# Kernel tuning notes

Measured on AMD Instinct MI355X. Metric: run time of the kernel, lower is better.

Reference implementation:

```python
import jax, jax.numpy as jnp
import numpy as np

B, N, D, P = 32, 16, 64, 8  # batch, num_objs, in_feat_dim, patch size
PAIRS = N * (N - 1)


def _conv_relu(x, W, b):
    # Conv2d(kernel=3, stride=1, padding=1) + ReLU, NCHW/OIHW layout
    y = jax.lax.conv_general_dilated(
        x, W, window_strides=(1, 1), padding='SAME',
        dimension_numbers=('NCHW', 'OIHW', 'NCHW'))
    return jax.nn.relu(y + b[None, :, None, None])


def setup_inputs() -> dict:
    key = jax.random.key(0)
    ks = jax.random.split(key, 12)
    x = jax.random.normal(ks[0], (B, N, D, P, P), jnp.float32)
    # g_idx: cols 0,1 index into the repeated pair axis of size N*(N-1); col 2 is a 0/1 mask
    i0 = jax.random.randint(ks[1], (B, PAIRS, 1), 0, PAIRS)
    i1 = jax.random.randint(ks[2], (B, PAIRS, 1), 0, PAIRS)
    m = jax.random.randint(ks[3], (B, PAIRS, 1), 0, 2)
    g_idx = jnp.concatenate([i0, i1, m], axis=2)

    def w(k, o, i):
        return jax.random.normal(k, (o, i, 3, 3), jnp.float32) * (1.0 / np.sqrt(i * 9.0))

    return {
        'x': x, 'g_idx': g_idx,
        'W_rel': w(ks[4], D, 2 * D), 'b_rel': jnp.zeros((D,), jnp.float32),
        'W_self': w(ks[5], D, D), 'b_self': jnp.zeros((D,), jnp.float32),
        'W_aff': w(ks[6], D, D), 'b_aff': jnp.zeros((D,), jnp.float32),
        'W_agg': w(ks[7], D, 2 * D), 'b_agg': jnp.zeros((D,), jnp.float32),
    }


def reference(x, g_idx, W_rel, b_rel, W_self, b_self, W_aff, b_aff, W_agg, b_agg):
    b, n, d, p, _ = x.shape
    pairs = n * (n - 1)
    s = x
    # x1: [B, N*(N-1), D, P, P]
    x1 = jnp.tile(x, (1, n - 1, 1, 1, 1))

    def gather_pair(col):
        idx = g_idx[:, :, col][:, :, None, None, None]  # [B, pairs, 1, 1, 1]
        idx = jnp.broadcast_to(idx, (b, pairs, d, p, p))
        return jnp.take_along_axis(x1, idx, axis=1)

    y1 = gather_pair(0)
    y2 = gather_pair(1)
    mask = g_idx[:, :, 2][:, :, None, None, None].astype(x.dtype)
    r = jnp.concatenate([y1, y2], axis=2) * mask  # [B, pairs, 2D, P, P]
    r = _conv_relu(r.reshape(-1, 2 * d, p, p), W_rel, b_rel)
    r = r.reshape(b, n, n - 1, d, p, p).sum(axis=2)  # scatter-sum per object

    xs = _conv_relu(x.reshape(-1, d, p, p), W_self, b_self).reshape(b, n, d, p, p)
    pred = xs + r
    a = _conv_relu(pred.reshape(-1, d, p, p), W_aff, b_aff).reshape(b, n, d, p, p)
    a = jnp.concatenate([a, s], axis=2)  # [B, N, 2D, P, P]
    out = _conv_relu(a.reshape(-1, 2 * d, p, p), W_agg, b_agg).reshape(b, n, d, p, p)
    return out
```

## Files before the change

kernel.cpp:

```cpp
#include <hip/hip_runtime.h>


#define NIMG 512
#define IMGSZ 4096

using bf16x8 = __attribute__((ext_vector_type(8))) short;
using f32x4  = __attribute__((ext_vector_type(4))) float;

__device__ inline unsigned short f2bf(float f) {
  union { float f; unsigned u; } v; v.f = f;
  unsigned r = v.u + 0x7fffu + ((v.u >> 16) & 1u);
  return (unsigned short)(r >> 16);
}

__device__ inline f32x4 bf4_to_f32(uint2 p) {
  union { unsigned u; float f; } c;
  f32x4 r;
  c.u = (p.x & 0xffffu) << 16;  r[0] = c.f;
  c.u = (p.x & 0xffff0000u);    r[1] = c.f;
  c.u = (p.y & 0xffffu) << 16;  r[2] = c.f;
  c.u = (p.y & 0xffff0000u);    r[3] = c.f;
  return r;
}

__global__ __launch_bounds__(256) void prep_w(
    const float* __restrict__ Wr, const float* __restrict__ Ws,
    const float* __restrict__ Wa, const float* __restrict__ Wg,
    unsigned short* __restrict__ Wt)
{
  int i4 = (blockIdx.x * 256 + threadIdx.x) * 4;
  if (i4 >= 221184) return;
  unsigned short o4[4];
#pragma unroll
  for (int e = 0; e < 4; ++e) {
    int idx = i4 + e;
    float v;
    if (idx < 73728) {
      int c = idx / 36864, r = idx % 36864;
      int t = r >> 12, oc = (r >> 6) & 63, ic = r & 63;
      v = (c == 0 ? Ws : Wa)[oc * 576 + ic * 9 + t];
    } else {
      int r2 = idx - 73728;
      int half = r2 / 73728, rr = r2 % 73728;
      int t = rr >> 13, oc = (rr >> 7) & 63, ic = rr & 127;
      v = (half ? Wg : Wr)[oc * 1152 + ic * 9 + t];
    }
    o4[e] = f2bf(v);
  }
  uint2 pk;
  pk.x = (unsigned)o4[0] | ((unsigned)o4[1] << 16);
  pk.y = (unsigned)o4[2] | ((unsigned)o4[3] << 16);
  *(uint2*)(Wt + i4) = pk;
}

__device__ inline void decode_img(int j, int& b, int& o) {
  b = ((j >> 7) << 3) | (j & 7);
  o = (j >> 3) & 15;
}

template<int ROWX>
__device__ inline void stage_x512(const float* __restrict__ xb,
                                  unsigned short* __restrict__ s,
                                  int coff, int w8, int px) {
#pragma unroll
  for (int r = 0; r < 4; ++r) {
    int ic0 = (w8 + 8 * r) * 2;
    const float* sp = xb + ic0 * 64;
    float a = sp[px], c = sp[64 + px];
    *(unsigned*)(s + px * ROWX + coff + ic0) =
        (unsigned)f2bf(a) | ((unsigned)f2bf(c) << 16);
  }
}

__global__ __launch_bounds__(512, 4) void k1(
    const float* __restrict__ x,
    const unsigned short* __restrict__ Wt,
    unsigned short* __restrict__ cA, unsigned short* __restrict__ cB)
{
  constexpr int ROW = 72;
  __shared__ __align__(16) unsigned short sX[65 * ROW];
  int b, o;
  decode_img(blockIdx.x, b, o);
  const int img = b * 16 + o;
  const int tid = threadIdx.x;
  const int w8 = tid >> 6, lane = tid & 63;

  stage_x512<ROW>(x + (size_t)img * IMGSZ, sX, 0, w8, lane);
  if (tid < 36) ((unsigned*)(sX + 64 * ROW))[tid] = 0;
  __syncthreads();

  const int half = tid >> 8;
  const int w = w8 & 3;
  const int q = lane >> 4, n16 = lane & 15;
  const int ocb = w * 16;
  const int co = ocb + q * 4;

  int pyt[4], pxt[4];
#pragma unroll
  for (int t = 0; t < 4; ++t) { int p = t * 16 + n16; pyt[t] = p >> 3; pxt[t] = p & 7; }

  f32x4 acc[4] = {};
  const unsigned short* WH = Wt + 73728 + (ocb + n16) * 128 + q * 8 + half * 64;
#pragma unroll
  for (int tap = 0; tap < 9; ++tap) {
    const int dy = tap / 3 - 1, dx = tap % 3 - 1;
    int spt[4];
#pragma unroll
    for (int t = 0; t < 4; ++t) {
      int sy = pyt[t] + dy, sx = pxt[t] + dx;
      spt[t] = ((unsigned)sy < 8u && (unsigned)sx < 8u) ? (sy * 8 + sx) : 64;
    }
#pragma unroll
    for (int ks = 0; ks < 2; ++ks) {
      bf16x8 aa = *(const bf16x8*)(WH + tap * 8192 + ks * 32);
#pragma unroll
      for (int t = 0; t < 4; ++t) {
        bf16x8 bt = *(const bf16x8*)(sX + spt[t] * ROW + ks * 32 + q * 8);
        acc[t] = __builtin_amdgcn_mfma_f32_16x16x32_bf16(aa, bt, acc[t], 0, 0, 0);
      }
    }
  }

  unsigned short* dst = half ? cB : cA;
  const size_t ib = (size_t)img * IMGSZ;
#pragma unroll
  for (int t = 0; t < 4; ++t) {
    int p = t * 16 + n16;
    uint2 pa;
    pa.x = (unsigned)f2bf(acc[t][0]) | ((unsigned)f2bf(acc[t][1]) << 16);
    pa.y = (unsigned)f2bf(acc[t][2]) | ((unsigned)f2bf(acc[t][3]) << 16);
    *(uint2*)(dst + ib + p * 64 + co) = pa;
  }
}

__global__ __launch_bounds__(512, 4) void k2(
    const float* __restrict__ x,
    const int* __restrict__ g_idx,
    const unsigned short* __restrict__ Wt,
    const float* __restrict__ b_rel, const float* __restrict__ b_self,
    const float* __restrict__ b_aff, const float* __restrict__ b_agg,
    const unsigned short* __restrict__ cA, const unsigned short* __restrict__ cB,
    float* __restrict__ out)
{
  constexpr int ROW = 72, ROW2 = 136, XROW = 68;
  __shared__ __align__(16) unsigned short sX[65 * ROW2];
  __shared__ __align__(16) unsigned short sPred[65 * ROW];
  __shared__ __align__(16) float sXS[64 * XROW];
  __shared__ int so1a[16], so2a[16];
  __shared__ float sma[16];
  __shared__ int s_na;

  int b, i;
  decode_img(blockIdx.x, b, i);
  const int img = b * 16 + i;
  const int tid = threadIdx.x;
  const int w8 = tid >> 6, lane = tid & 63;

  int o1v = 0, o2v = 0, mv = 0;
  if (tid < 15) {
    const int* gp = g_idx + ((size_t)b * 240 + i * 15 + tid) * 3;
    o1v = gp[0] & 15;
    o2v = gp[1] & 15;
    mv  = gp[2];
  }
  if (tid < 64) {
    if (tid < 16) { so1a[tid] = 0; so2a[tid] = 0; sma[tid] = 0.f; }
    unsigned long long mk = __ballot(mv != 0);
    int pfx = (int)__popcll(mk & ((1ull << tid) - 1));
    if (mv) { so1a[pfx] = o1v; so2a[pfx] = o2v; sma[pfx] = 1.f; }
    if (tid == 0) s_na = (int)__popcll(mk);
  }

  stage_x512<ROW2>(x + (size_t)img * IMGSZ, sX, 64, w8, lane);
  if (tid < 68) ((unsigned*)(sX + 64 * ROW2))[tid] = 0;
  if (tid < 36) ((unsigned*)(sPred + 64 * ROW))[tid] = 0;
  __syncthreads();

  const int w = w8 & 3;
  const int q = lane >> 4, n16 = lane & 15;
  const int ocb = w * 16;
  const int co = ocb + q * 4;
  const int aw64  = (ocb + n16) * 64 + q * 8;
  const int aw128 = (ocb + n16) * 128 + q * 8;

  int pyt[4], pxt[4];
#pragma unroll
  for (int t = 0; t < 4; ++t) { int p = t * 16 + n16; pyt[t] = p >> 3; pxt[t] = p & 7; }

  if (tid < 256) {
    f32x4 f[4] = {};
    const unsigned short* WS = Wt + aw64;
#pragma unroll
    for (int tap = 0; tap < 9; ++tap) {
      const int dy = tap / 3 - 1, dx = tap % 3 - 1;
      int spt[4];
#pragma unroll
      for (int t = 0; t < 4; ++t) {
        int sy = pyt[t] + dy, sx = pxt[t] + dx;
        spt[t] = ((unsigned)sy < 8u && (unsigned)sx < 8u) ? (sy * 8 + sx) : 64;
      }
#pragma unroll
      for (int ks = 0; ks < 2; ++ks) {
        bf16x8 a = *(const bf16x8*)(WS + tap * 4096 + ks * 32);
#pragma unroll
        for (int t = 0; t < 4; ++t) {
          bf16x8 bt = *(const bf16x8*)(sX + spt[t] * ROW2 + 64 + ks * 32 + q * 8);
          f[t] = __builtin_amdgcn_mfma_f32_16x16x32_bf16(a, bt, f[t], 0, 0, 0);
        }
      }
    }
#pragma unroll
    for (int t = 0; t < 4; ++t) {
      int p = t * 16 + n16;
      f32x4 vs = f[t];
#pragma unroll
      for (int r = 0; r < 4; ++r) vs[r] = fmaxf(vs[r] + b_self[co + r], 0.f);
      *(f32x4*)(sXS + p * XROW + co) = vs;
    }
  }
  __syncthreads();

  {
    const size_t bb = (size_t)b * 16 * IMGSZ;
    const int na = s_na;
    const int nc = (na + 3) >> 2;
    const float c0 = (float)(15 - na);
#pragma unroll 1
    for (int pass = 0; pass < 2; ++pass) {
      const int e = tid * 4 + pass * 2048;
      const int e_px = e >> 6, e_ic = e & 63;
      f32x4 xv = *(const f32x4*)(sXS + e_px * XROW + e_ic);
      float acc[4], br[4];
#pragma unroll
      for (int r = 0; r < 4; ++r) {
        br[r] = b_rel[e_ic + r];
        acc[r] = xv[r] + c0 * fmaxf(br[r], 0.f);
      }
#pragma unroll 1
      for (int c = 0; c < nc; ++c) {
        uint2 v1[4], v2[4];
#pragma unroll
        for (int jj = 0; jj < 4; ++jj) {
          int j = c * 4 + jj;
          v1[jj] = *(const uint2*)(cA + bb + (size_t)so1a[j] * IMGSZ + e);
          v2[jj] = *(const uint2*)(cB + bb + (size_t)so2a[j] * IMGSZ + e);
        }
#pragma unroll
        for (int jj = 0; jj < 4; ++jj) {
          float s = sma[c * 4 + jj];
          f32x4 a1 = bf4_to_f32(v1[jj]);
          f32x4 a2 = bf4_to_f32(v2[jj]);
#pragma unroll
          for (int r = 0; r < 4; ++r)
            acc[r] += s * fmaxf(a1[r] + a2[r] + br[r], 0.f);
        }
      }
      uint2 pk;
      pk.x = (unsigned)f2bf(acc[0]) | ((unsigned)f2bf(acc[1]) << 16);
      pk.y = (unsigned)f2bf(acc[2]) | ((unsigned)f2bf(acc[3]) << 16);
      *(uint2*)(sPred + e_px * ROW + e_ic) = pk;
    }
  }
  __syncthreads();

  if (tid < 256) {
    f32x4 f[4] = {};
    const unsigned short* WA = Wt + 36864 + aw64;
#pragma unroll
    for (int tap = 0; tap < 9; ++tap) {
      const int dy = tap / 3 - 1, dx = tap % 3 - 1;
      int spt[4];
#pragma unroll
      for (int t = 0; t < 4; ++t) {
        int sy = pyt[t] + dy, sx = pxt[t] + dx;
        spt[t] = ((unsigned)sy < 8u && (unsigned)sx < 8u) ? (sy * 8 + sx) : 64;
      }
#pragma unroll
      for (int ks = 0; ks < 2; ++ks) {
        bf16x8 a = *(const bf16x8*)(WA + tap * 4096 + ks * 32);
#pragma unroll
        for (int t = 0; t < 4; ++t) {
          bf16x8 bt = *(const bf16x8*)(sPred + spt[t] * ROW + ks * 32 + q * 8);
          f[t] = __builtin_amdgcn_mfma_f32_16x16x32_bf16(a, bt, f[t], 0, 0, 0);
        }
      }
    }
#pragma unroll
    for (int t = 0; t < 4; ++t) {
      int p = t * 16 + n16;
      float v0 = fmaxf(f[t][0] + b_aff[co + 0], 0.f);
      float v1 = fmaxf(f[t][1] + b_aff[co + 1], 0.f);
      float v2 = fmaxf(f[t][2] + b_aff[co + 2], 0.f);
      float v3 = fmaxf(f[t][3] + b_aff[co + 3], 0.f);
      uint2 pk;
      pk.x = (unsigned)f2bf(v0) | ((unsigned)f2bf(v1) << 16);
      pk.y = (unsigned)f2bf(v2) | ((unsigned)f2bf(v3) << 16);
      *(uint2*)(sX + p * ROW2 + co) = pk;
    }
  }
  __syncthreads();

  if (tid < 256) {
    f32x4 g[4] = {};
    const unsigned short* WG = Wt + 147456 + aw128;
#pragma unroll
    for (int tap = 0; tap < 9; ++tap) {
      const int dy = tap / 3 - 1, dx = tap % 3 - 1;
      int spt[4];
#pragma unroll
      for (int t = 0; t < 4; ++t) {
        int sy = pyt[t] + dy, sx = pxt[t] + dx;
        spt[t] = ((unsigned)sy < 8u && (unsigned)sx < 8u) ? (sy * 8 + sx) : 64;
      }
#pragma unroll
      for (int ks = 0; ks < 4; ++ks) {
        bf16x8 a = *(const bf16x8*)(WG + tap * 8192 + ks * 32);
#pragma unroll
        for (int t = 0; t < 4; ++t) {
          bf16x8 bt = *(const bf16x8*)(sX + spt[t] * ROW2 + ks * 32 + q * 8);
          g[t] = __builtin_amdgcn_mfma_f32_16x16x32_bf16(bt, a, g[t], 0, 0, 0);
        }
      }
    }
    float* ob = out + (size_t)img * IMGSZ;
    const float bg = b_agg[ocb + n16];
#pragma unroll
    for (int t = 0; t < 4; ++t) {
      f32x4 v;
#pragma unroll
      for (int r = 0; r < 4; ++r) v[r] = fmaxf(g[t][r] + bg, 0.f);
      *(f32x4*)(ob + (ocb + n16) * 64 + t * 16 + q * 4) = v;
    }
  }
}

extern "C" void kernel_launch(void* const* d_in, const int* in_sizes, int n_in,
                              void* d_out, int out_size, void* d_ws, size_t ws_size,
                              hipStream_t stream) {
  const float* x      = (const float*)d_in[0];
  const int*   g_idx  = (const int*)  d_in[1];
  const float* W_rel  = (const float*)d_in[2];
  const float* b_rel  = (const float*)d_in[3];
  const float* W_self = (const float*)d_in[4];
  const float* b_self = (const float*)d_in[5];
  const float* W_aff  = (const float*)d_in[6];
  const float* b_aff  = (const float*)d_in[7];
  const float* W_agg  = (const float*)d_in[8];
  const float* b_agg  = (const float*)d_in[9];
  float* out = (float*)d_out;

  unsigned short* cA = (unsigned short*)d_ws;
  unsigned short* cB = cA + 2097152;
  unsigned short* Wt = cB + 2097152;

  prep_w<<<216, 256, 0, stream>>>(W_rel, W_self, W_aff, W_agg, Wt);
  k1<<<NIMG, 512, 0, stream>>>(x, Wt, cA, cB);
  k2<<<NIMG, 512, 0, stream>>>(x, g_idx, Wt, b_rel, b_self, b_aff, b_agg,
                               cA, cB, out);
}
```

Baseline: 116.2 us.

## Move self-conv into k1 split across both halves and prefetch first-tap weights

The W_self convolution moves from k2, where only 256 threads ran it serially before the aggregation, into k1. In k1 all 512 threads share it by splitting the input channels between the two halves and reducing the partial sums through shared memory. The result is written to a new fp32 workspace buffer that k2 reads from global memory instead of computing. Separately, first-tap weight fragments are loaded before the staging barriers to hide their latency. This shortens k2's critical path but adds a 2 MB fp32 global round trip, extra shared memory in k1, and another barrier.

```diff
diff --git a/kernel.cpp b/kernel.cpp
--- a/kernel.cpp
+++ b/kernel.cpp
@@ -75,32 +75,39 @@
 __global__ __launch_bounds__(512, 4) void k1(
     const float* __restrict__ x,
     const unsigned short* __restrict__ Wt,
-    unsigned short* __restrict__ cA, unsigned short* __restrict__ cB)
+    const float* __restrict__ b_self,
+    unsigned short* __restrict__ cA, unsigned short* __restrict__ cB,
+    float* __restrict__ xs)
 {
-  constexpr int ROW = 72;
+  constexpr int ROW = 72, PROW = 68;
   __shared__ __align__(16) unsigned short sX[65 * ROW];
+  __shared__ __align__(16) float sPart[64 * PROW];
   int b, o;
   decode_img(blockIdx.x, b, o);
   const int img = b * 16 + o;
   const int tid = threadIdx.x;
   const int w8 = tid >> 6, lane = tid & 63;
-
-  stage_x512<ROW>(x + (size_t)img * IMGSZ, sX, 0, w8, lane);
-  if (tid < 36) ((unsigned*)(sX + 64 * ROW))[tid] = 0;
-  __syncthreads();
-
   const int half = tid >> 8;
   const int w = w8 & 3;
   const int q = lane >> 4, n16 = lane & 15;
   const int ocb = w * 16;
   const int co = ocb + q * 4;
 
+  const unsigned short* WH = Wt + 73728 + (ocb + n16) * 128 + q * 8 + half * 64;
+  const unsigned short* WS = Wt + (ocb + n16) * 64 + q * 8 + half * 32;
+  bf16x8 wp0 = *(const bf16x8*)(WH);
+  bf16x8 wp1 = *(const bf16x8*)(WH + 32);
+  bf16x8 wpS = *(const bf16x8*)(WS);
+
+  stage_x512<ROW>(x + (size_t)img * IMGSZ, sX, 0, w8, lane);
+  if (tid < 36) ((unsigned*)(sX + 64 * ROW))[tid] = 0;
+  __syncthreads();
+
   int pyt[4], pxt[4];
 #pragma unroll
   for (int t = 0; t < 4; ++t) { int p = t * 16 + n16; pyt[t] = p >> 3; pxt[t] = p & 7; }
 
-  f32x4 acc[4] = {};
-  const unsigned short* WH = Wt + 73728 + (ocb + n16) * 128 + q * 8 + half * 64;
+  f32x4 acc[4] = {}, sf[4] = {};
 #pragma unroll
   for (int tap = 0; tap < 9; ++tap) {
     const int dy = tap / 3 - 1, dx = tap % 3 - 1;
@@ -112,12 +119,19 @@
     }
 #pragma unroll
     for (int ks = 0; ks < 2; ++ks) {
-      bf16x8 aa = *(const bf16x8*)(WH + tap * 8192 + ks * 32);
+      bf16x8 aa = (tap == 0) ? (ks == 0 ? wp0 : wp1)
+                             : *(const bf16x8*)(WH + tap * 8192 + ks * 32);
 #pragma unroll
       for (int t = 0; t < 4; ++t) {
         bf16x8 bt = *(const bf16x8*)(sX + spt[t] * ROW + ks * 32 + q * 8);
         acc[t] = __builtin_amdgcn_mfma_f32_16x16x32_bf16(aa, bt, acc[t], 0, 0, 0);
       }
+    }
+    bf16x8 as = (tap == 0) ? wpS : *(const bf16x8*)(WS + tap * 4096);
+#pragma unroll
+    for (int t = 0; t < 4; ++t) {
+      bf16x8 bts = *(const bf16x8*)(sX + spt[t] * ROW + half * 32 + q * 8);
+      sf[t] = __builtin_amdgcn_mfma_f32_16x16x32_bf16(as, bts, sf[t], 0, 0, 0);
     }
   }
 
@@ -131,21 +145,41 @@
     pa.y = (unsigned)f2bf(acc[t][2]) | ((unsigned)f2bf(acc[t][3]) << 16);
     *(uint2*)(dst + ib + p * 64 + co) = pa;
   }
+
+  if (half) {
+#pragma unroll
+    for (int t = 0; t < 4; ++t)
+      *(f32x4*)(sPart + (t * 16 + n16) * PROW + co) = sf[t];
+  }
+  __syncthreads();
+  if (!half) {
+    float* xb = xs + (size_t)img * IMGSZ;
+#pragma unroll
+    for (int t = 0; t < 4; ++t) {
+      int p = t * 16 + n16;
+      f32x4 o2 = *(const f32x4*)(sPart + p * PROW + co);
+      f32x4 v;
+#pragma unroll
+      for (int r = 0; r < 4; ++r)
+        v[r] = fmaxf(sf[t][r] + o2[r] + b_self[co + r], 0.f);
+      *(f32x4*)(xb + p * 64 + co) = v;
+    }
+  }
 }
 
 __global__ __launch_bounds__(512, 4) void k2(
     const float* __restrict__ x,
     const int* __restrict__ g_idx,
     const unsigned short* __restrict__ Wt,
-    const float* __restrict__ b_rel, const float* __restrict__ b_self,
+    const float* __restrict__ b_rel,
     const float* __restrict__ b_aff, const float* __restrict__ b_agg,
     const unsigned short* __restrict__ cA, const unsigned short* __restrict__ cB,
+    const float* __restrict__ xs,
     float* __restrict__ out)
 {
-  constexpr int ROW = 72, ROW2 = 136, XROW = 68;
+  constexpr int ROW = 72, ROW2 = 136;
   __shared__ __align__(16) unsigned short sX[65 * ROW2];
   __shared__ __align__(16) unsigned short sPred[65 * ROW];
-  __shared__ __align__(16) float sXS[64 * XROW];
   __shared__ int so1a[16], so2a[16];
   __shared__ float sma[16];
   __shared__ int s_na;
@@ -187,38 +221,9 @@
 #pragma unroll
   for (int t = 0; t < 4; ++t) { int p = t * 16 + n16; pyt[t] = p >> 3; pxt[t] = p & 7; }
 
-  if (tid < 256) {
-    f32x4 f[4] = {};
-    const unsigned short* WS = Wt + aw64;
-#pragma unroll
-    for (int tap = 0; tap < 9; ++tap) {
-      const int dy = tap / 3 - 1, dx = tap % 3 - 1;
-      int spt[4];
-#pragma unroll
-      for (int t = 0; t < 4; ++t) {
-        int sy = pyt[t] + dy, sx = pxt[t] + dx;
-        spt[t] = ((unsigned)sy < 8u && (unsigned)sx < 8u) ? (sy * 8 + sx) : 64;
-      }
-#pragma unroll
-      for (int ks = 0; ks < 2; ++ks) {
-        bf16x8 a = *(const bf16x8*)(WS + tap * 4096 + ks * 32);
-#pragma unroll
-        for (int t = 0; t < 4; ++t) {
-          bf16x8 bt = *(const bf16x8*)(sX + spt[t] * ROW2 + 64 + ks * 32 + q * 8);
-          f[t] = __builtin_amdgcn_mfma_f32_16x16x32_bf16(a, bt, f[t], 0, 0, 0);
-        }
-      }
-    }
-#pragma unroll
-    for (int t = 0; t < 4; ++t) {
-      int p = t * 16 + n16;
-      f32x4 vs = f[t];
-#pragma unroll
-      for (int r = 0; r < 4; ++r) vs[r] = fmaxf(vs[r] + b_self[co + r], 0.f);
-      *(f32x4*)(sXS + p * XROW + co) = vs;
-    }
-  }
-  __syncthreads();
+  const unsigned short* WAp = Wt + 36864 + aw64;
+  bf16x8 ap0 = *(const bf16x8*)(WAp);
+  bf16x8 ap1 = *(const bf16x8*)(WAp + 32);
 
   {
     const size_t bb = (size_t)b * 16 * IMGSZ;
@@ -229,7 +234,7 @@
     for (int pass = 0; pass < 2; ++pass) {
       const int e = tid * 4 + pass * 2048;
       const int e_px = e >> 6, e_ic = e & 63;
-      f32x4 xv = *(const f32x4*)(sXS + e_px * XROW + e_ic);
+      f32x4 xv = *(const f32x4*)(xs + (size_t)img * IMGSZ + e);
       float acc[4], br[4];
 #pragma unroll
       for (int r = 0; r < 4; ++r) {
@@ -263,9 +268,12 @@
   }
   __syncthreads();
 
+  const unsigned short* WGp = Wt + 147456 + aw128;
+  bf16x8 gp0 = *(const bf16x8*)(WGp);
+  bf16x8 gp1 = *(const bf16x8*)(WGp + 32);
+
   if (tid < 256) {
     f32x4 f[4] = {};
-    const unsigned short* WA = Wt + 36864 + aw64;
 #pragma unroll
     for (int tap = 0; tap < 9; ++tap) {
       const int dy = tap / 3 - 1, dx = tap % 3 - 1;
@@ -277,7 +285,8 @@
       }
 #pragma unroll
       for (int ks = 0; ks < 2; ++ks) {
-        bf16x8 a = *(const bf16x8*)(WA + tap * 4096 + ks * 32);
+        bf16x8 a = (tap == 0) ? (ks == 0 ? ap0 : ap1)
+                              : *(const bf16x8*)(WAp + tap * 4096 + ks * 32);
 #pragma unroll
         for (int t = 0; t < 4; ++t) {
           bf16x8 bt = *(const bf16x8*)(sPred + spt[t] * ROW + ks * 32 + q * 8);
@@ -302,7 +311,6 @@
 
   if (tid < 256) {
     f32x4 g[4] = {};
-    const unsigned short* WG = Wt + 147456 + aw128;
 #pragma unroll
     for (int tap = 0; tap < 9; ++tap) {
       const int dy = tap / 3 - 1, dx = tap % 3 - 1;
@@ -314,7 +322,9 @@
       }
 #pragma unroll
       for (int ks = 0; ks < 4; ++ks) {
-        bf16x8 a = *(const bf16x8*)(WG + tap * 8192 + ks * 32);
+        bf16x8 a = (tap == 0 && ks < 2)
+                       ? (ks == 0 ? gp0 : gp1)
+                       : *(const bf16x8*)(WGp + tap * 8192 + ks * 32);
 #pragma unroll
         for (int t = 0; t < 4; ++t) {
           bf16x8 bt = *(const bf16x8*)(sX + spt[t] * ROW2 + ks * 32 + q * 8);
@@ -352,9 +362,10 @@
   unsigned short* cA = (unsigned short*)d_ws;
   unsigned short* cB = cA + 2097152;
   unsigned short* Wt = cB + 2097152;
+  float* xs = (float*)(Wt + 221184);
 
   prep_w<<<216, 256, 0, stream>>>(W_rel, W_self, W_aff, W_agg, Wt);
-  k1<<<NIMG, 512, 0, stream>>>(x, Wt, cA, cB);
-  k2<<<NIMG, 512, 0, stream>>>(x, g_idx, Wt, b_rel, b_self, b_aff, b_agg,
-                               cA, cB, out);
-}
+  k1<<<NIMG, 512, 0, stream>>>(x, Wt, b_self, cA, cB, xs);
+  k2<<<NIMG, 512, 0, stream>>>(x, g_idx, Wt, b_rel, b_aff, b_agg,
+                               cA, cB, xs, out);
+}
```

Result: slower. 119.9 us (+3.2%).

## Split conv work across all waves, fold weight prep into k1, prefetch weights

Applied to the files above, without the earlier changes.

The self, aff and agg convolutions in k2 now run on all 8 waves, each handling two of the four pixel tiles, where before only 4 waves worked and the rest sat idle. k1 moves to 1024 threads, likewise splitting pixel tiles across twice as many waves. Conversion of the self, aff and agg weights moves out of the separate prep kernel into k1, leaving a smaller prep kernel for W_rel only. The first-tap weight fragments are loaded ahead of barriers to hide latency. The cost is more duplicated weight loads per block and a heavier k1 block, whose 1024-thread size may cut occupancy.

```diff
diff --git a/kernel.cpp b/kernel.cpp
--- a/kernel.cpp
+++ b/kernel.cpp
@@ -23,34 +23,22 @@
   return r;
 }
 
-__global__ __launch_bounds__(256) void prep_w(
-    const float* __restrict__ Wr, const float* __restrict__ Ws,
-    const float* __restrict__ Wa, const float* __restrict__ Wg,
-    unsigned short* __restrict__ Wt)
+__global__ __launch_bounds__(256) void prep_rel(
+    const float* __restrict__ Wr, unsigned short* __restrict__ Wt)
 {
   int i4 = (blockIdx.x * 256 + threadIdx.x) * 4;
-  if (i4 >= 221184) return;
+  if (i4 >= 73728) return;
   unsigned short o4[4];
 #pragma unroll
-  for (int e = 0; e < 4; ++e) {
-    int idx = i4 + e;
-    float v;
-    if (idx < 73728) {
-      int c = idx / 36864, r = idx % 36864;
-      int t = r >> 12, oc = (r >> 6) & 63, ic = r & 63;
-      v = (c == 0 ? Ws : Wa)[oc * 576 + ic * 9 + t];
-    } else {
-      int r2 = idx - 73728;
-      int half = r2 / 73728, rr = r2 % 73728;
-      int t = rr >> 13, oc = (rr >> 7) & 63, ic = rr & 127;
-      v = (half ? Wg : Wr)[oc * 1152 + ic * 9 + t];
-    }
-    o4[e] = f2bf(v);
+  for (int k = 0; k < 4; ++k) {
+    int idx = i4 + k;
+    int t = idx >> 13, oc = (idx >> 7) & 63, ic = idx & 127;
+    o4[k] = f2bf(Wr[oc * 1152 + ic * 9 + t]);
   }
   uint2 pk;
   pk.x = (unsigned)o4[0] | ((unsigned)o4[1] << 16);
   pk.y = (unsigned)o4[2] | ((unsigned)o4[3] << 16);
-  *(uint2*)(Wt + i4) = pk;
+  *(uint2*)(Wt + 73728 + i4) = pk;
 }
 
 __device__ inline void decode_img(int j, int& b, int& o) {
@@ -72,9 +60,25 @@
   }
 }
 
-__global__ __launch_bounds__(512, 4) void k1(
+template<int ROWX>
+__device__ inline void stage_x1024(const float* __restrict__ xb,
+                                   unsigned short* __restrict__ s,
+                                   int w16, int px) {
+#pragma unroll
+  for (int r = 0; r < 2; ++r) {
+    int ic0 = (w16 + 16 * r) * 2;
+    const float* sp = xb + ic0 * 64;
+    float a = sp[px], c = sp[64 + px];
+    *(unsigned*)(s + px * ROWX + ic0) =
+        (unsigned)f2bf(a) | ((unsigned)f2bf(c) << 16);
+  }
+}
+
+__global__ __launch_bounds__(1024, 4) void k1(
     const float* __restrict__ x,
-    const unsigned short* __restrict__ Wt,
+    const float* __restrict__ Ws, const float* __restrict__ Wa,
+    const float* __restrict__ Wg,
+    unsigned short* __restrict__ Wt,
     unsigned short* __restrict__ cA, unsigned short* __restrict__ cB)
 {
   constexpr int ROW = 72;
@@ -83,40 +87,72 @@
   decode_img(blockIdx.x, b, o);
   const int img = b * 16 + o;
   const int tid = threadIdx.x;
-  const int w8 = tid >> 6, lane = tid & 63;
-
-  stage_x512<ROW>(x + (size_t)img * IMGSZ, sX, 0, w8, lane);
-  if (tid < 36) ((unsigned*)(sX + 64 * ROW))[tid] = 0;
-  __syncthreads();
-
-  const int half = tid >> 8;
-  const int w = w8 & 3;
+  const int w16 = tid >> 6, lane = tid & 63;
+  const int half = w16 >> 3;
+  const int th   = (w16 >> 2) & 1;
+  const int w    = w16 & 3;
   const int q = lane >> 4, n16 = lane & 15;
   const int ocb = w * 16;
   const int co = ocb + q * 4;
 
-  int pyt[4], pxt[4];
-#pragma unroll
-  for (int t = 0; t < 4; ++t) { int p = t * 16 + n16; pyt[t] = p >> 3; pxt[t] = p & 7; }
-
-  f32x4 acc[4] = {};
   const unsigned short* WH = Wt + 73728 + (ocb + n16) * 128 + q * 8 + half * 64;
+  bf16x8 wp0 = *(const bf16x8*)(WH);
+  bf16x8 wp1 = *(const bf16x8*)(WH + 32);
+
+  stage_x1024<ROW>(x + (size_t)img * IMGSZ, sX, w16, lane);
+  if (tid < 36) ((unsigned*)(sX + 64 * ROW))[tid] = 0;
+
+  if (tid < 72) {
+    int e4 = blockIdx.x * 288 + tid * 4;
+    unsigned short o4[4];
+#pragma unroll
+    for (int k = 0; k < 4; ++k) {
+      int e = e4 + k;
+      float v;
+      if (e < 73728) {
+        int c = e / 36864, r = e % 36864;
+        int t = r >> 12, oc = (r >> 6) & 63, ic = r & 63;
+        v = (c == 0 ? Ws : Wa)[oc * 576 + ic * 9 + t];
+      } else {
+        int rr = e - 73728;
+        int t = rr >> 13, oc = (rr >> 7) & 63, ic = rr & 127;
+        v = Wg[oc * 1152 + ic * 9 + t];
+      }
+      o4[k] = f2bf(v);
+    }
+    int we = (e4 < 73728) ? e4 : e4 + 73728;
+    uint2 pk;
+    pk.x = (unsigned)o4[0] | ((unsigned)o4[1] << 16);
+    pk.y = (unsigned)o4[2] | ((unsigned)o4[3] << 16);
+    *(uint2*)(Wt + we) = pk;
+  }
+  __syncthreads();
+
+  int pyt[2], pxt[2];
+#pragma unroll
+  for (int t2 = 0; t2 < 2; ++t2) {
+    int p = (th * 2 + t2) * 16 + n16;
+    pyt[t2] = p >> 3; pxt[t2] = p & 7;
+  }
+
+  f32x4 acc[2] = {};
 #pragma unroll
   for (int tap = 0; tap < 9; ++tap) {
     const int dy = tap / 3 - 1, dx = tap % 3 - 1;
-    int spt[4];
-#pragma unroll
-    for (int t = 0; t < 4; ++t) {
-      int sy = pyt[t] + dy, sx = pxt[t] + dx;
-      spt[t] = ((unsigned)sy < 8u && (unsigned)sx < 8u) ? (sy * 8 + sx) : 64;
+    int spt[2];
+#pragma unroll
+    for (int t2 = 0; t2 < 2; ++t2) {
+      int sy = pyt[t2] + dy, sx = pxt[t2] + dx;
+      spt[t2] = ((unsigned)sy < 8u && (unsigned)sx < 8u) ? (sy * 8 + sx) : 64;
     }
 #pragma unroll
     for (int ks = 0; ks < 2; ++ks) {
-      bf16x8 aa = *(const bf16x8*)(WH + tap * 8192 + ks * 32);
-#pragma unroll
-      for (int t = 0; t < 4; ++t) {
-        bf16x8 bt = *(const bf16x8*)(sX + spt[t] * ROW + ks * 32 + q * 8);
-        acc[t] = __builtin_amdgcn_mfma_f32_16x16x32_bf16(aa, bt, acc[t], 0, 0, 0);
+      bf16x8 aa = (tap == 0) ? (ks == 0 ? wp0 : wp1)
+                             : *(const bf16x8*)(WH + tap * 8192 + ks * 32);
+#pragma unroll
+      for (int t2 = 0; t2 < 2; ++t2) {
+        bf16x8 bt = *(const bf16x8*)(sX + spt[t2] * ROW + ks * 32 + q * 8);
+        acc[t2] = __builtin_amdgcn_mfma_f32_16x16x32_bf16(aa, bt, acc[t2], 0, 0, 0);
       }
     }
   }
@@ -124,11 +160,11 @@
   unsigned short* dst = half ? cB : cA;
   const size_t ib = (size_t)img * IMGSZ;
 #pragma unroll
-  for (int t = 0; t < 4; ++t) {
-    int p = t * 16 + n16;
+  for (int t2 = 0; t2 < 2; ++t2) {
+    int p = (th * 2 + t2) * 16 + n16;
     uint2 pa;
-    pa.x = (unsigned)f2bf(acc[t][0]) | ((unsigned)f2bf(acc[t][1]) << 16);
-    pa.y = (unsigned)f2bf(acc[t][2]) | ((unsigned)f2bf(acc[t][3]) << 16);
+    pa.x = (unsigned)f2bf(acc[t2][0]) | ((unsigned)f2bf(acc[t2][1]) << 16);
+    pa.y = (unsigned)f2bf(acc[t2][2]) | ((unsigned)f2bf(acc[t2][3]) << 16);
     *(uint2*)(dst + ib + p * 64 + co) = pa;
   }
 }
@@ -176,49 +212,57 @@
   if (tid < 36) ((unsigned*)(sPred + 64 * ROW))[tid] = 0;
   __syncthreads();
 
-  const int w = w8 & 3;
+  const int w  = w8 & 3;
+  const int th = w8 >> 2;
   const int q = lane >> 4, n16 = lane & 15;
   const int ocb = w * 16;
   const int co = ocb + q * 4;
   const int aw64  = (ocb + n16) * 64 + q * 8;
   const int aw128 = (ocb + n16) * 128 + q * 8;
 
-  int pyt[4], pxt[4];
-#pragma unroll
-  for (int t = 0; t < 4; ++t) { int p = t * 16 + n16; pyt[t] = p >> 3; pxt[t] = p & 7; }
-
-  if (tid < 256) {
-    f32x4 f[4] = {};
+  int pyt[2], pxt[2];
+#pragma unroll
+  for (int t2 = 0; t2 < 2; ++t2) {
+    int p = (th * 2 + t2) * 16 + n16;
+    pyt[t2] = p >> 3; pxt[t2] = p & 7;
+  }
+
+  {
+    f32x4 f[2] = {};
     const unsigned short* WS = Wt + aw64;
 #pragma unroll
     for (int tap = 0; tap < 9; ++tap) {
       const int dy = tap / 3 - 1, dx = tap % 3 - 1;
-      int spt[4];
-#pragma unroll
-      for (int t = 0; t < 4; ++t) {
-        int sy = pyt[t] + dy, sx = pxt[t] + dx;
-        spt[t] = ((unsigned)sy < 8u && (unsigned)sx < 8u) ? (sy * 8 + sx) : 64;
+      int spt[2];
+#pragma unroll
+      for (int t2 = 0; t2 < 2; ++t2) {
+        int sy = pyt[t2] + dy, sx = pxt[t2] + dx;
+        spt[t2] = ((unsigned)sy < 8u && (unsigned)sx < 8u) ? (sy * 8 + sx) : 64;
       }
 #pragma unroll
       for (int ks = 0; ks < 2; ++ks) {
         bf16x8 a = *(const bf16x8*)(WS + tap * 4096 + ks * 32);
 #pragma unroll
-        for (int t = 0; t < 4; ++t) {
-          bf16x8 bt = *(const bf16x8*)(sX + spt[t] * ROW2 + 64 + ks * 32 + q * 8);
-          f[t] = __builtin_amdgcn_mfma_f32_16x16x32_bf16(a, bt, f[t], 0, 0, 0);
+        for (int t2 = 0; t2 < 2; ++t2) {
+          bf16x8 bt = *(const bf16x8*)(sX + spt[t2] * ROW2 + 64 + ks * 32 + q * 8);
+          f[t2] = __builtin_amdgcn_mfma_f32_16x16x32_bf16(a, bt, f[t2], 0, 0, 0);
         }
       }
     }
 #pragma unroll
-    for (int t = 0; t < 4; ++t) {
-      int p = t * 16 + n16;
-      f32x4 vs = f[t];
+    for (int t2 = 0; t2 < 2; ++t2) {
+      int p = (th * 2 + t2) * 16 + n16;
+      f32x4 vs = f[t2];
 #pragma unroll
       for (int r = 0; r < 4; ++r) vs[r] = fmaxf(vs[r] + b_self[co + r], 0.f);
       *(f32x4*)(sXS + p * XROW + co) = vs;
     }
   }
   __syncthreads();
+
+  const unsigned short* WAp = Wt + 36864 + aw64;
+  bf16x8 ap0 = *(const bf16x8*)(WAp);
+  bf16x8 ap1 = *(const bf16x8*)(WAp + 32);
 
   {
     const size_t bb = (size_t)b * 16 * IMGSZ;
@@ -263,35 +307,39 @@
   }
   __syncthreads();
 
-  if (tid < 256) {
-    f32x4 f[4] = {};
-    const unsigned short* WA = Wt + 36864 + aw64;
+  const unsigned short* WGp = Wt + 147456 + aw128;
+  bf16x8 gp0 = *(const bf16x8*)(WGp);
+  bf16x8 gp1 = *(const bf16x8*)(WGp + 32);
+
+  {
+    f32x4 f[2] = {};
 #pragma unroll
     for (int tap = 0; tap < 9; ++tap) {
       const int dy = tap / 3 - 1, dx = tap % 3 - 1;
-      int spt[4];
-#pragma unroll
-      for (int t = 0; t < 4; ++t) {
-        int sy = pyt[t] + dy, sx = pxt[t] + dx;
-        spt[t] = ((unsigned)sy < 8u && (unsigned)sx < 8u) ? (sy * 8 + sx) : 64;
+      int spt[2];
+#pragma unroll
+      for (int t2 = 0; t2 < 2; ++t2) {
+        int sy = pyt[t2] + dy, sx = pxt[t2] + dx;
+        spt[t2] = ((unsigned)sy < 8u && (unsigned)sx < 8u) ? (sy * 8 + sx) : 64;
       }
 #pragma unroll
       for (int ks = 0; ks < 2; ++ks) {
-        bf16x8 a = *(const bf16x8*)(WA + tap * 4096 + ks * 32);
-#pragma unroll
-        for (int t = 0; t < 4; ++t) {
-          bf16x8 bt = *(const bf16x8*)(sPred + spt[t] * ROW + ks * 32 + q * 8);
-          f[t] = __builtin_amdgcn_mfma_f32_16x16x32_bf16(a, bt, f[t], 0, 0, 0);
+        bf16x8 a = (tap == 0) ? (ks == 0 ? ap0 : ap1)
+                              : *(const bf16x8*)(WAp + tap * 4096 + ks * 32);
+#pragma unroll
+        for (int t2 = 0; t2 < 2; ++t2) {
+          bf16x8 bt = *(const bf16x8*)(sPred + spt[t2] * ROW + ks * 32 + q * 8);
+          f[t2] = __builtin_amdgcn_mfma_f32_16x16x32_bf16(a, bt, f[t2], 0, 0, 0);
         }
       }
     }
 #pragma unroll
-    for (int t = 0; t < 4; ++t) {
-      int p = t * 16 + n16;
-      float v0 = fmaxf(f[t][0] + b_aff[co + 0], 0.f);
-      float v1 = fmaxf(f[t][1] + b_aff[co + 1], 0.f);
-      float v2 = fmaxf(f[t][2] + b_aff[co + 2], 0.f);
-      float v3 = fmaxf(f[t][3] + b_aff[co + 3], 0.f);
+    for (int t2 = 0; t2 < 2; ++t2) {
+      int p = (th * 2 + t2) * 16 + n16;
+      float v0 = fmaxf(f[t2][0] + b_aff[co + 0], 0.f);
+      float v1 = fmaxf(f[t2][1] + b_aff[co + 1], 0.f);
+      float v2 = fmaxf(f[t2][2] + b_aff[co + 2], 0.f);
+      float v3 = fmaxf(f[t2][3] + b_aff[co + 3], 0.f);
       uint2 pk;
       pk.x = (unsigned)f2bf(v0) | ((unsigned)f2bf(v1) << 16);
       pk.y = (unsigned)f2bf(v2) | ((unsigned)f2bf(v3) << 16);
@@ -300,35 +348,37 @@
   }
   __syncthreads();
 
-  if (tid < 256) {
-    f32x4 g[4] = {};
-    const unsigned short* WG = Wt + 147456 + aw128;
+  {
+    f32x4 g[2] = {};
 #pragma unroll
     for (int tap = 0; tap < 9; ++tap) {
       const int dy = tap / 3 - 1, dx = tap % 3 - 1;
-      int spt[4];
-#pragma unroll
-      for (int t = 0; t < 4; ++t) {
-        int sy = pyt[t] + dy, sx = pxt[t] + dx;
-        spt[t] = ((unsigned)sy < 8u && (unsigned)sx < 8u) ? (sy * 8 + sx) : 64;
+      int spt[2];
+#pragma unroll
+      for (int t2 = 0; t2 < 2; ++t2) {
+        int sy = pyt[t2] + dy, sx = pxt[t2] + dx;
+        spt[t2] = ((unsigned)sy < 8u && (unsigned)sx < 8u) ? (sy * 8 + sx) : 64;
       }
 #pragma unroll
       for (int ks = 0; ks < 4; ++ks) {
-        bf16x8 a = *(const bf16x8*)(WG + tap * 8192 + ks * 32);
-#pragma unroll
-        for (int t = 0; t < 4; ++t) {
-          bf16x8 bt = *(const bf16x8*)(sX + spt[t] * ROW2 + ks * 32 + q * 8);
-          g[t] = __builtin_amdgcn_mfma_f32_16x16x32_bf16(bt, a, g[t], 0, 0, 0);
+        bf16x8 a = (tap == 0 && ks < 2)
+                       ? (ks == 0 ? gp0 : gp1)
+                       : *(const bf16x8*)(WGp + tap * 8192 + ks * 32);
+#pragma unroll
+        for (int t2 = 0; t2 < 2; ++t2) {
+          bf16x8 bt = *(const bf16x8*)(sX + spt[t2] * ROW2 + ks * 32 + q * 8);
+          g[t2] = __builtin_amdgcn_mfma_f32_16x16x32_bf16(bt, a, g[t2], 0, 0, 0);
         }
       }
     }
     float* ob = out + (size_t)img * IMGSZ;
     const float bg = b_agg[ocb + n16];
 #pragma unroll
-    for (int t = 0; t < 4; ++t) {
+    for (int t2 = 0; t2 < 2; ++t2) {
+      int t = th * 2 + t2;
       f32x4 v;
 #pragma unroll
-      for (int r = 0; r < 4; ++r) v[r] = fmaxf(g[t][r] + bg, 0.f);
+      for (int r = 0; r < 4; ++r) v[r] = fmaxf(g[t2][r] + bg, 0.f);
       *(f32x4*)(ob + (ocb + n16) * 64 + t * 16 + q * 4) = v;
     }
   }
@@ -353,8 +403,8 @@
   unsigned short* cB = cA + 2097152;
   unsigned short* Wt = cB + 2097152;
 
-  prep_w<<<216, 256, 0, stream>>>(W_rel, W_self, W_aff, W_agg, Wt);
-  k1<<<NIMG, 512, 0, stream>>>(x, Wt, cA, cB);
+  prep_rel<<<72, 256, 0, stream>>>(W_rel, Wt);
+  k1<<<NIMG, 1024, 0, stream>>>(x, W_self, W_aff, W_agg, Wt, cA, cB);
   k2<<<NIMG, 512, 0, stream>>>(x, g_idx, Wt, b_rel, b_self, b_aff, b_agg,
                                cA, cB, out);
 }
```

Measured after the change: 137.6 us. 18.5% more time.

## Fuse relation conv into main kernel, convolving gathered pairs directly

Applied to the files above, without the earlier changes.

Drops the separate k1 kernel, which precomputed per-object half-convolutions of W_rel into global bf16 buffers, and the global-memory gather of those results. The fused kernel instead stages each active pair's two object images into shared memory and runs the full 128-channel relation conv with MFMA. The two 256-thread groups handle alternating pairs, and their partial sums are combined through shared memory. This removes one launch and the intermediate global round-trip, but the relation conv now costs about twice the MFMA work per active pair, and the extra pair buffers use more LDS per block.

```diff
diff --git a/kernel.cpp b/kernel.cpp
--- a/kernel.cpp
+++ b/kernel.cpp
@@ -11,16 +11,6 @@
   union { float f; unsigned u; } v; v.f = f;
   unsigned r = v.u + 0x7fffu + ((v.u >> 16) & 1u);
   return (unsigned short)(r >> 16);
-}
-
-__device__ inline f32x4 bf4_to_f32(uint2 p) {
-  union { unsigned u; float f; } c;
-  f32x4 r;
-  c.u = (p.x & 0xffffu) << 16;  r[0] = c.f;
-  c.u = (p.x & 0xffff0000u);    r[1] = c.f;
-  c.u = (p.y & 0xffffu) << 16;  r[2] = c.f;
-  c.u = (p.y & 0xffff0000u);    r[3] = c.f;
-  return r;
 }
 
 __global__ __launch_bounds__(256) void prep_w(
@@ -72,89 +62,51 @@
   }
 }
 
-__global__ __launch_bounds__(512, 4) void k1(
-    const float* __restrict__ x,
-    const unsigned short* __restrict__ Wt,
-    unsigned short* __restrict__ cA, unsigned short* __restrict__ cB)
-{
-  constexpr int ROW = 72;
-  __shared__ __align__(16) unsigned short sX[65 * ROW];
-  int b, o;
-  decode_img(blockIdx.x, b, o);
-  const int img = b * 16 + o;
-  const int tid = threadIdx.x;
-  const int w8 = tid >> 6, lane = tid & 63;
-
-  stage_x512<ROW>(x + (size_t)img * IMGSZ, sX, 0, w8, lane);
-  if (tid < 36) ((unsigned*)(sX + 64 * ROW))[tid] = 0;
-  __syncthreads();
-
-  const int half = tid >> 8;
-  const int w = w8 & 3;
-  const int q = lane >> 4, n16 = lane & 15;
-  const int ocb = w * 16;
-  const int co = ocb + q * 4;
-
-  int pyt[4], pxt[4];
-#pragma unroll
-  for (int t = 0; t < 4; ++t) { int p = t * 16 + n16; pyt[t] = p >> 3; pxt[t] = p & 7; }
-
-  f32x4 acc[4] = {};
-  const unsigned short* WH = Wt + 73728 + (ocb + n16) * 128 + q * 8 + half * 64;
-#pragma unroll
-  for (int tap = 0; tap < 9; ++tap) {
-    const int dy = tap / 3 - 1, dx = tap % 3 - 1;
-    int spt[4];
-#pragma unroll
-    for (int t = 0; t < 4; ++t) {
-      int sy = pyt[t] + dy, sx = pxt[t] + dx;
-      spt[t] = ((unsigned)sy < 8u && (unsigned)sx < 8u) ? (sy * 8 + sx) : 64;
-    }
-#pragma unroll
-    for (int ks = 0; ks < 2; ++ks) {
-      bf16x8 aa = *(const bf16x8*)(WH + tap * 8192 + ks * 32);
-#pragma unroll
-      for (int t = 0; t < 4; ++t) {
-        bf16x8 bt = *(const bf16x8*)(sX + spt[t] * ROW + ks * 32 + q * 8);
-        acc[t] = __builtin_amdgcn_mfma_f32_16x16x32_bf16(aa, bt, acc[t], 0, 0, 0);
-      }
-    }
-  }
-
-  unsigned short* dst = half ? cB : cA;
-  const size_t ib = (size_t)img * IMGSZ;
-#pragma unroll
-  for (int t = 0; t < 4; ++t) {
-    int p = t * 16 + n16;
-    uint2 pa;
-    pa.x = (unsigned)f2bf(acc[t][0]) | ((unsigned)f2bf(acc[t][1]) << 16);
-    pa.y = (unsigned)f2bf(acc[t][2]) | ((unsigned)f2bf(acc[t][3]) << 16);
-    *(uint2*)(dst + ib + p * 64 + co) = pa;
-  }
-}
-
-__global__ __launch_bounds__(512, 4) void k2(
+__device__ inline void stage_pair(const float* __restrict__ x1,
+                                  const float* __restrict__ x2,
+                                  unsigned short* __restrict__ buf,
+                                  int w4, int px) {
+#pragma unroll
+  for (int r = 0; r < 8; ++r) {
+    int ic0 = (w4 + 4 * r) * 2;
+    const float* sp = x1 + ic0 * 64;
+    float a = sp[px], c = sp[64 + px];
+    *(unsigned*)(buf + px * 136 + ic0) =
+        (unsigned)f2bf(a) | ((unsigned)f2bf(c) << 16);
+  }
+#pragma unroll
+  for (int r = 0; r < 8; ++r) {
+    int ic0 = (w4 + 4 * r) * 2;
+    const float* sp = x2 + ic0 * 64;
+    float a = sp[px], c = sp[64 + px];
+    *(unsigned*)(buf + px * 136 + 64 + ic0) =
+        (unsigned)f2bf(a) | ((unsigned)f2bf(c) << 16);
+  }
+}
+
+__global__ __launch_bounds__(512, 4) void kmain(
     const float* __restrict__ x,
     const int* __restrict__ g_idx,
     const unsigned short* __restrict__ Wt,
     const float* __restrict__ b_rel, const float* __restrict__ b_self,
     const float* __restrict__ b_aff, const float* __restrict__ b_agg,
-    const unsigned short* __restrict__ cA, const unsigned short* __restrict__ cB,
     float* __restrict__ out)
 {
-  constexpr int ROW = 72, ROW2 = 136, XROW = 68;
+  constexpr int ROW = 72, ROW2 = 136;
   __shared__ __align__(16) unsigned short sX[65 * ROW2];
   __shared__ __align__(16) unsigned short sPred[65 * ROW];
-  __shared__ __align__(16) float sXS[64 * XROW];
+  __shared__ __align__(16) unsigned short sPair[2][65 * ROW2];
   __shared__ int so1a[16], so2a[16];
-  __shared__ float sma[16];
   __shared__ int s_na;
 
   int b, i;
   decode_img(blockIdx.x, b, i);
   const int img = b * 16 + i;
   const int tid = threadIdx.x;
+  const int grp = tid >> 8;
   const int w8 = tid >> 6, lane = tid & 63;
+  const int w4 = w8 & 3;
+  const float* xbase = x + (size_t)b * 16 * IMGSZ;
 
   int o1v = 0, o2v = 0, mv = 0;
   if (tid < 15) {
@@ -164,21 +116,24 @@
     mv  = gp[2];
   }
   if (tid < 64) {
-    if (tid < 16) { so1a[tid] = 0; so2a[tid] = 0; sma[tid] = 0.f; }
     unsigned long long mk = __ballot(mv != 0);
     int pfx = (int)__popcll(mk & ((1ull << tid) - 1));
-    if (mv) { so1a[pfx] = o1v; so2a[pfx] = o2v; sma[pfx] = 1.f; }
+    if (mv) { so1a[pfx] = o1v; so2a[pfx] = o2v; }
     if (tid == 0) s_na = (int)__popcll(mk);
   }
 
   stage_x512<ROW2>(x + (size_t)img * IMGSZ, sX, 64, w8, lane);
   if (tid < 68) ((unsigned*)(sX + 64 * ROW2))[tid] = 0;
   if (tid < 36) ((unsigned*)(sPred + 64 * ROW))[tid] = 0;
+  if (tid < 136) {
+    int g = tid / 68, c = tid % 68;
+    ((unsigned*)(sPair[g] + 64 * ROW2))[c] = 0;
+  }
   __syncthreads();
 
-  const int w = w8 & 3;
+  const int na = s_na;
   const int q = lane >> 4, n16 = lane & 15;
-  const int ocb = w * 16;
+  const int ocb = w4 * 16;
   const int co = ocb + q * 4;
   const int aw64  = (ocb + n16) * 64 + q * 8;
   const int aw128 = (ocb + n16) * 128 + q * 8;
@@ -187,7 +142,13 @@
 #pragma unroll
   for (int t = 0; t < 4; ++t) { int p = t * 16 + n16; pyt[t] = p >> 3; pxt[t] = p & 7; }
 
-  if (tid < 256) {
+  float br4[4];
+#pragma unroll
+  for (int r = 0; r < 4; ++r) br4[r] = b_rel[co + r];
+
+  f32x4 pacc[4] = {};
+
+  if (!grp) {
     f32x4 f[4] = {};
     const unsigned short* WS = Wt + aw64;
 #pragma unroll
@@ -209,61 +170,83 @@
         }
       }
     }
-#pragma unroll
-    for (int t = 0; t < 4; ++t) {
-      int p = t * 16 + n16;
-      f32x4 vs = f[t];
-#pragma unroll
-      for (int r = 0; r < 4; ++r) vs[r] = fmaxf(vs[r] + b_self[co + r], 0.f);
-      *(f32x4*)(sXS + p * XROW + co) = vs;
+    const float c0 = (float)(15 - na);
+#pragma unroll
+    for (int t = 0; t < 4; ++t)
+#pragma unroll
+      for (int r = 0; r < 4; ++r)
+        pacc[t][r] = fmaxf(f[t][r] + b_self[co + r], 0.f)
+                   + c0 * fmaxf(br4[r], 0.f);
+  }
+
+  {
+    unsigned short* bufg = sPair[grp];
+    const unsigned short* WR = Wt + 73728 + aw128;
+    const int niter = (na + 1) >> 1;
+#pragma unroll 1
+    for (int it = 0; it < niter; ++it) {
+      const int jc = 2 * it + grp;
+      __syncthreads();
+      if (jc < na)
+        stage_pair(xbase + (size_t)so1a[jc] * IMGSZ,
+                   xbase + (size_t)so2a[jc] * IMGSZ, bufg, w4, lane);
+      __syncthreads();
+      if (jc < na) {
+        f32x4 pcc[4] = {};
+#pragma unroll
+        for (int tap = 0; tap < 9; ++tap) {
+          const int dy = tap / 3 - 1, dx = tap % 3 - 1;
+          int spt[4];
+#pragma unroll
+          for (int t = 0; t < 4; ++t) {
+            int sy = pyt[t] + dy, sx = pxt[t] + dx;
+            spt[t] = ((unsigned)sy < 8u && (unsigned)sx < 8u) ? (sy * 8 + sx) : 64;
+          }
+#pragma unroll
+          for (int ks = 0; ks < 4; ++ks) {
+            bf16x8 aa = *(const bf16x8*)(WR + tap * 8192 + ks * 32);
+#pragma unroll
+            for (int t = 0; t < 4; ++t) {
+              bf16x8 bt = *(const bf16x8*)(bufg + spt[t] * ROW2 + ks * 32 + q * 8);
+              pcc[t] = __builtin_amdgcn_mfma_f32_16x16x32_bf16(aa, bt, pcc[t], 0, 0, 0);
+            }
+          }
+        }
+#pragma unroll
+        for (int t = 0; t < 4; ++t)
+#pragma unroll
+          for (int r = 0; r < 4; ++r)
+            pacc[t][r] += fmaxf(pcc[t][r] + br4[r], 0.f);
+      }
     }
   }
   __syncthreads();
 
   {
-    const size_t bb = (size_t)b * 16 * IMGSZ;
-    const int na = s_na;
-    const int nc = (na + 3) >> 2;
-    const float c0 = (float)(15 - na);
-#pragma unroll 1
-    for (int pass = 0; pass < 2; ++pass) {
-      const int e = tid * 4 + pass * 2048;
-      const int e_px = e >> 6, e_ic = e & 63;
-      f32x4 xv = *(const f32x4*)(sXS + e_px * XROW + e_ic);
-      float acc[4], br[4];
-#pragma unroll
-      for (int r = 0; r < 4; ++r) {
-        br[r] = b_rel[e_ic + r];
-        acc[r] = xv[r] + c0 * fmaxf(br[r], 0.f);
-      }
-#pragma unroll 1
-      for (int c = 0; c < nc; ++c) {
-        uint2 v1[4], v2[4];
-#pragma unroll
-        for (int jj = 0; jj < 4; ++jj) {
-          int j = c * 4 + jj;
-          v1[jj] = *(const uint2*)(cA + bb + (size_t)so1a[j] * IMGSZ + e);
-          v2[jj] = *(const uint2*)(cB + bb + (size_t)so2a[j] * IMGSZ + e);
-        }
-#pragma unroll
-        for (int jj = 0; jj < 4; ++jj) {
-          float s = sma[c * 4 + jj];
-          f32x4 a1 = bf4_to_f32(v1[jj]);
-          f32x4 a2 = bf4_to_f32(v2[jj]);
-#pragma unroll
-          for (int r = 0; r < 4; ++r)
-            acc[r] += s * fmaxf(a1[r] + a2[r] + br[r], 0.f);
-        }
-      }
-      uint2 pk;
-      pk.x = (unsigned)f2bf(acc[0]) | ((unsigned)f2bf(acc[1]) << 16);
-      pk.y = (unsigned)f2bf(acc[2]) | ((unsigned)f2bf(acc[3]) << 16);
-      *(uint2*)(sPred + e_px * ROW + e_ic) = pk;
+    float* scr = (float*)sPair[0];
+    if (grp) {
+#pragma unroll
+      for (int t = 0; t < 4; ++t)
+        *(f32x4*)(scr + (t * 16 + n16) * 68 + co) = pacc[t];
+    }
+    __syncthreads();
+    if (!grp) {
+#pragma unroll
+      for (int t = 0; t < 4; ++t) {
+        int p = t * 16 + n16;
+        f32x4 o2 = *(const f32x4*)(scr + p * 68 + co);
+        float v0 = pacc[t][0] + o2[0], v1 = pacc[t][1] + o2[1];
+        float v2 = pacc[t][2] + o2[2], v3 = pacc[t][3] + o2[3];
+        uint2 pk;
+        pk.x = (unsigned)f2bf(v0) | ((unsigned)f2bf(v1) << 16);
+        pk.y = (unsigned)f2bf(v2) | ((unsigned)f2bf(v3) << 16);
+        *(uint2*)(sPred + p * ROW + co) = pk;
+      }
     }
   }
   __syncthreads();
 
-  if (tid < 256) {
+  if (!grp) {
     f32x4 f[4] = {};
     const unsigned short* WA = Wt + 36864 + aw64;
 #pragma unroll
@@ -300,7 +283,7 @@
   }
   __syncthreads();
 
-  if (tid < 256) {
+  if (!grp) {
     f32x4 g[4] = {};
     const unsigned short* WG = Wt + 147456 + aw128;
 #pragma unroll
@@ -349,12 +332,9 @@
   const float* b_agg  = (const float*)d_in[9];
   float* out = (float*)d_out;
 
-  unsigned short* cA = (unsigned short*)d_ws;
-  unsigned short* cB = cA + 2097152;
-  unsigned short* Wt = cB + 2097152;
+  unsigned short* Wt = (unsigned short*)d_ws;
 
   prep_w<<<216, 256, 0, stream>>>(W_rel, W_self, W_aff, W_agg, Wt);
-  k1<<<NIMG, 512, 0, stream>>>(x, Wt, cA, cB);
-  k2<<<NIMG, 512, 0, stream>>>(x, g_idx, Wt, b_rel, b_self, b_aff, b_agg,
-                               cA, cB, out);
-}
+  kmain<<<NIMG, 512, 0, stream>>>(x, g_idx, Wt, b_rel, b_self, b_aff, b_agg,
+                                  out);
+}
```

Result: slower. 262.8 us (+126.2%).
